# Performance work log

Measured on AMD Instinct MI355X. Metric: run time of the kernel, lower is better.

## Reference

```python
import jax, jax.numpy as jnp
import numpy as np

BIT, ROW, COL = 4, 8, 8
Y_ROW, Z_COL, K = 128, 128, 256  # inter_dimension = 256, K8 = 32
K8 = K // 8
BATCH, SEQ = 8, 2048


def _unpack_bits(packed, n_bits):
    """Unpack uint8 along last axis, big-endian (MSB first), matching np.packbits."""
    shifts = jnp.arange(7, -1, -1, dtype=jnp.uint8)
    bits = (packed[..., None] >> shifts) & jnp.uint8(1)  # [..., k8, 8]
    return bits.reshape(*packed.shape[:-1], -1)[..., :n_bits]


def setup_inputs() -> dict:
    rng = np.random.default_rng(0)
    # Generate underlying binary tensors so Y_sum / Z_sum are consistent with packed bits.
    Yb = rng.integers(0, 2, size=(BIT, ROW, COL, Y_ROW, K), dtype=np.uint8)
    Zb = rng.integers(0, 2, size=(BIT, ROW, COL, K, Z_COL), dtype=np.uint8)
    Y_packed = np.packbits(Yb, axis=-1)                                # [BIT,ROW,COL,Y_ROW,K8]
    Z_packed = np.packbits(Zb.transpose(0, 1, 2, 4, 3), axis=-1)        # [BIT,ROW,COL,Z_COL,K8]
    Y_sum = Yb.sum(axis=-1, keepdims=True).astype(np.int32)             # [BIT,ROW,COL,Y_ROW,1]
    Z_sum = Zb.sum(axis=-2, keepdims=True).astype(np.int32)             # [BIT,ROW,COL,1,Z_COL]

    key = jax.random.key(0)
    k1, k2, k3, k4, k5, k6 = jax.random.split(key, 6)
    X = jax.random.normal(k1, (BATCH, SEQ, COL * Z_COL), dtype=jnp.float32)
    a = jax.random.normal(k2, (BIT, 1, 1, 1, 1), dtype=jnp.float32) * 0.1
    b = jax.random.normal(k3, (BIT, 1, 1, 1, 1), dtype=jnp.float32) * 0.1
    c = jax.random.normal(k4, (BIT, 1, 1, 1, 1), dtype=jnp.float32) * 0.1
    d = jax.random.normal(k5, (1, 1, 1, 1), dtype=jnp.float32) * 0.1
    bias = jax.random.normal(k6, (ROW * Y_ROW,), dtype=jnp.float32) * 0.1
    return {
        "X": X,
        "Y_packed": jnp.asarray(Y_packed),
        "Z_packed": jnp.asarray(Z_packed),
        "Y_sum": jnp.asarray(Y_sum),
        "Z_sum": jnp.asarray(Z_sum),
        "a": a, "b": b, "c": c, "d": d, "bias": bias,
    }


def reference(X, Y_packed, Z_packed, Y_sum, Z_sum, a, b, c, d, bias):
    dtype = X.dtype
    # Unpack bits (fallback path of _matmul_via_unpack) and do binary matmul.
    Y = _unpack_bits(Y_packed, K).astype(dtype)        # [BIT,ROW,COL,Y_ROW,K]
    Zt = _unpack_bits(Z_packed, K).astype(dtype)       # [BIT,ROW,COL,Z_COL,K]
    W_core = jnp.einsum('brcyk,brczk->brcyz', Y, Zt)   # [BIT,ROW,COL,Y_ROW,Z_COL]
    # Affine recombination over bit planes.
    W = a * W_core + b * Y_sum.astype(dtype) + c * Z_sum.astype(dtype)
    W = W.sum(axis=0) + d                               # [ROW,COL,Y_ROW,Z_COL]
    W = W.transpose(0, 2, 1, 3).reshape(ROW * Y_ROW, COL * Z_COL)
    return X @ W.T + bias
```

## Files before the change

### kernel.cpp

```cpp
#include <hip/hip_runtime.h>
#include <hip/hip_bf16.h>
#include <stdint.h>

typedef unsigned int u32;
typedef unsigned short u16;
typedef __attribute__((ext_vector_type(8))) short short8;
typedef __attribute__((ext_vector_type(4))) float floatx4;

#define N_DIM 1024
#define K_DIM 1024
#define M_DIM 16384
#define EPW  68

__device__ __forceinline__ u32 pack4(uint4 v) {
    return (v.x & 0xffu) | ((v.y & 0xffu) << 8) | ((v.z & 0xffu) << 16) | (v.w << 24);
}

__device__ __forceinline__ u16 bf16rne(float f) {
    u32 u = __float_as_uint(f);
    return (u16)((u + 0x7fffu + ((u >> 16) & 1u)) >> 16);
}

__device__ __forceinline__ void load16_lds(const void* g, void* l) {
    __builtin_amdgcn_global_load_lds(
        (const __attribute__((address_space(1))) void*)g,
        (__attribute__((address_space(3))) void*)l, 16, 0, 0);
}

__global__ __launch_bounds__(256) void build_w(
        const u32* __restrict__ yp, const u32* __restrict__ zp,
        const int* __restrict__ ysum, const int* __restrict__ zsum,
        const float* __restrict__ pa, const float* __restrict__ pb,
        const float* __restrict__ pc, const float* __restrict__ pd,
        __hip_bfloat16* __restrict__ Wb) {
    __shared__ u32 sY[4096];
    __shared__ u32 sZ[1024];
    __shared__ int sYs[512];
    __shared__ int sZs[128];

    const int tid = threadIdx.x;
    const int rc = blockIdx.x >> 2;
    const int zq = blockIdx.x & 3;
    const int r = rc >> 3, c = rc & 7;
    const int z0 = zq * 32;

    const uint4 d0 = ((const uint4*)yp)[0], d1 = ((const uint4*)yp)[1];
    const int sdet = __popc(d0.x) + __popc(d0.y) + __popc(d0.z) + __popc(d0.w)
                   + __popc(d1.x) + __popc(d1.y) + __popc(d1.z) + __popc(d1.w);
    const bool widened = (sdet != ysum[0]);

    if (!widened) {
#pragma unroll
        for (int j = 0; j < 4; ++j) {
            const int chunk = tid + j * 256;
            const int f = chunk * 4;
            const int bit = f >> 10, rem = f & 1023;
            const u32 gw = (u32)((bit * 64 + r * 8 + c) * 1024 + rem);
            ((uint4*)sY)[chunk] = *(const uint4*)(yp + gw);
        }
        {
            const int f = tid * 4;
            const int bit = f >> 8;
            const u32 gw = (u32)((bit * 64 + r * 8 + c) * 1024 + z0 * 8 + (f & 255));
            ((uint4*)sZ)[tid] = *(const uint4*)(zp + gw);
        }
    } else {
#pragma unroll
        for (int j = 0; j < 4; ++j) {
            const int chunk = tid + j * 256;
            const int f = chunk * 4;
            const int bit = f >> 10, rem = f & 1023;
            const u32 gw = (u32)((bit * 64 + r * 8 + c) * 1024 + rem);
            uint4 o;
            o.x = pack4(((const uint4*)yp)[gw + 0]);
            o.y = pack4(((const uint4*)yp)[gw + 1]);
            o.z = pack4(((const uint4*)yp)[gw + 2]);
            o.w = pack4(((const uint4*)yp)[gw + 3]);
            ((uint4*)sY)[chunk] = o;
        }
        {
            const int f = tid * 4;
            const int bit = f >> 8;
            const u32 gw = (u32)((bit * 64 + r * 8 + c) * 1024 + z0 * 8 + (f & 255));
            uint4 o;
            o.x = pack4(((const uint4*)zp)[gw + 0]);
            o.y = pack4(((const uint4*)zp)[gw + 1]);
            o.z = pack4(((const uint4*)zp)[gw + 2]);
            o.w = pack4(((const uint4*)zp)[gw + 3]);
            ((uint4*)sZ)[tid] = o;
        }
    }
    for (int j = tid; j < 512; j += 256) {
        const int bit = j >> 7, y = j & 127;
        sYs[j] = ysum[((bit * 8 + r) * 8 + c) * 128 + y];
    }
    if (tid < 128) {
        const int bit = tid >> 5, zl = tid & 31;
        sZs[tid] = zsum[((bit * 8 + r) * 8 + c) * 128 + z0 + zl];
    }
    __syncthreads();

    float av[4], bv[4], cv[4];
#pragma unroll
    for (int bit = 0; bit < 4; ++bit) { av[bit] = pa[bit]; bv[bit] = pb[bit]; cv[bit] = pc[bit]; }
    const float dv = pd[0];

    const int y = tid & 127;
    const int zh = tid >> 7;

    u32 yw[4][8];
    float base = dv;
#pragma unroll
    for (int bit = 0; bit < 4; ++bit) {
        const uint4 q0 = ((const uint4*)sY)[bit * 256 + y * 2];
        const uint4 q1 = ((const uint4*)sY)[bit * 256 + y * 2 + 1];
        yw[bit][0] = q0.x; yw[bit][1] = q0.y; yw[bit][2] = q0.z; yw[bit][3] = q0.w;
        yw[bit][4] = q1.x; yw[bit][5] = q1.y; yw[bit][6] = q1.z; yw[bit][7] = q1.w;
        base += bv[bit] * (float)sYs[bit * 128 + y];
    }

    const int m = r * 128 + y;
#pragma unroll
    for (int zl2 = 0; zl2 < 16; ++zl2) {
        const int zl = zh * 16 + zl2;
        float wv = base;
#pragma unroll
        for (int bit = 0; bit < 4; ++bit) {
            const uint4 zw0 = ((const uint4*)sZ)[bit * 64 + zl * 2];
            const uint4 zw1 = ((const uint4*)sZ)[bit * 64 + zl * 2 + 1];
            int p = 0;
            p += __popc(yw[bit][0] & zw0.x);
            p += __popc(yw[bit][1] & zw0.y);
            p += __popc(yw[bit][2] & zw0.z);
            p += __popc(yw[bit][3] & zw0.w);
            p += __popc(yw[bit][4] & zw1.x);
            p += __popc(yw[bit][5] & zw1.y);
            p += __popc(yw[bit][6] & zw1.z);
            p += __popc(yw[bit][7] & zw1.w);
            wv += av[bit] * (float)p + cv[bit] * (float)sZs[bit * 32 + zl];
        }
        const int k = c * 128 + z0 + zl;
        Wb[(size_t)m * K_DIM + k] = __float2bfloat16(wv);
    }
}

__global__ __launch_bounds__(256) void convert_x(const float4* __restrict__ X,
                                                 ushort4* __restrict__ Xb) {
    const size_t base = (size_t)blockIdx.x * 512;
    const int tid = threadIdx.x;
    const float4 a = X[base + tid];
    const float4 b = X[base + 256 + tid];
    ushort4 oa, ob;
    oa.x = bf16rne(a.x); oa.y = bf16rne(a.y); oa.z = bf16rne(a.z); oa.w = bf16rne(a.w);
    ob.x = bf16rne(b.x); ob.y = bf16rne(b.y); ob.z = bf16rne(b.z); ob.w = bf16rne(b.w);
    Xb[base + tid] = oa;
    Xb[base + 256 + tid] = ob;
}

__global__ __launch_bounds__(512, 4) void gemm_bias(
        const u16* __restrict__ Xb, const u16* __restrict__ Wb,
        const float* __restrict__ bias, float* __restrict__ out) {
    __shared__ char lds[49152];
    char* As = lds;
    char* Bs = lds + 32768;

    const int tid = threadIdx.x;
    const int lane = tid & 63;
    const int w = tid >> 6;
    const int wr = w >> 1;
    const int wc = w & 1;
    const int mtile = blockIdx.x;
    const int ntile = blockIdx.y;
    const int m0 = mtile * 256, n0 = ntile * 128;

    const int lrow = lane >> 3;
    const int lkc  = (lane & 7) ^ lrow;
    const int fm = lane & 15, fq = lane >> 4;
    const int cx0 = ((0 + fq) ^ (fm & 7)) * 16;
    const int cx1 = ((4 + fq) ^ (fm & 7)) * 16;

    floatx4 acc[4][4] = {};

    for (int kt = 0; kt < K_DIM / 64; ++kt) {
        __syncthreads();
#pragma unroll
        for (int j = 0; j < 4; ++j) {
            const int cw = j * 8 + w;
            const int row = cw * 8 + lrow;
            load16_lds(Xb + (size_t)(m0 + row) * K_DIM + kt * 64 + lkc * 8,
                       As + cw * 1024 + lane * 16);
        }
#pragma unroll
        for (int j = 0; j < 2; ++j) {
            const int cw = j * 8 + w;
            const int row = cw * 8 + lrow;
            load16_lds(Wb + (size_t)(n0 + row) * K_DIM + kt * 64 + lkc * 8,
                       Bs + cw * 1024 + lane * 16);
        }
        __syncthreads();

#pragma unroll
        for (int kk = 0; kk < 2; ++kk) {
            const int cx = kk ? cx1 : cx0;
            short8 afr[4], bfr[4];
#pragma unroll
            for (int mi = 0; mi < 4; ++mi)
                afr[mi] = *(const short8*)(As + (wr * 64 + mi * 16 + fm) * 128 + cx);
#pragma unroll
            for (int ni = 0; ni < 4; ++ni)
                bfr[ni] = *(const short8*)(Bs + (wc * 64 + ni * 16 + fm) * 128 + cx);
#pragma unroll
            for (int mi = 0; mi < 4; ++mi)
#pragma unroll
                for (int ni = 0; ni < 4; ++ni)
                    acc[mi][ni] = __builtin_amdgcn_mfma_f32_16x16x32_bf16(
                        afr[mi], bfr[ni], acc[mi][ni], 0, 0, 0);
        }
    }

    float bias_r[4];
#pragma unroll
    for (int ni = 0; ni < 4; ++ni)
        bias_r[ni] = bias[n0 + wc * 64 + ni * 16 + fm];

    __syncthreads();
    float* ep = (float*)lds + w * (16 * EPW);
    const int gm0 = m0 + wr * 64;
    const int gn0 = n0 + wc * 64;

#pragma unroll
    for (int mi = 0; mi < 4; ++mi) {
#pragma unroll
        for (int ni = 0; ni < 4; ++ni)
#pragma unroll
            for (int reg = 0; reg < 4; ++reg)
                ep[(fq * 4 + reg) * EPW + ni * 16 + fm] = acc[mi][ni][reg] + bias_r[ni];
#pragma unroll
        for (int t = 0; t < 4; ++t) {
            const int lr = t * 4 + fq;
            const float4 v = *(const float4*)(ep + lr * EPW + fm * 4);
            *(float4*)(out + (size_t)(gm0 + mi * 16 + lr) * N_DIM + gn0 + fm * 4) = v;
        }
    }
}

extern "C" void kernel_launch(void* const* d_in, const int* in_sizes, int n_in,
                              void* d_out, int out_size, void* d_ws, size_t ws_size,
                              hipStream_t stream) {
    const float* X   = (const float*)d_in[0];
    const u32*   Yp  = (const u32*)d_in[1];
    const u32*   Zp  = (const u32*)d_in[2];
    const int*   Ys  = (const int*)d_in[3];
    const int*   Zs  = (const int*)d_in[4];
    const float* pa  = (const float*)d_in[5];
    const float* pb  = (const float*)d_in[6];
    const float* pc  = (const float*)d_in[7];
    const float* pd  = (const float*)d_in[8];
    const float* bias = (const float*)d_in[9];
    float* out = (float*)d_out;

    char* ws = (char*)d_ws;
    __hip_bfloat16* Wb = (__hip_bfloat16*)ws;
    u16*            Xb = (u16*)(ws + (2u << 20));

    build_w<<<256, 256, 0, stream>>>(Yp, Zp, Ys, Zs, pa, pb, pc, pd, Wb);
    convert_x<<<8192, 256, 0, stream>>>((const float4*)X, (ushort4*)Xb);
    gemm_bias<<<dim3(64, 8), 512, 0, stream>>>(Xb, (const u16*)Wb, bias, out);
}
```

Before: 172.3 us.

## Enlarge GEMM tile to 256x256 and double-buffer LDS with async prefetch

The GEMM block tile grows from 256x128 to 256x256, so each wave computes a 128x64 sub-tile with 32 accumulators. K-tiles are now double-buffered in 128 KB of dynamic LDS, with the next tile's global-to-LDS loads issued while the current one is being computed. The aim is more operand reuse per load and hidden global memory latency. The cost is higher register and LDS use, which limits occupancy to about one block per CU, and only 256 blocks are launched.

```diff
diff --git a/kernel.cpp b/kernel.cpp
--- a/kernel.cpp
+++ b/kernel.cpp
@@ -157,21 +157,18 @@
     Xb[base + 256 + tid] = ob;
 }
 
-__global__ __launch_bounds__(512, 4) void gemm_bias(
+__global__ __launch_bounds__(512, 2) void gemm_bias(
         const u16* __restrict__ Xb, const u16* __restrict__ Wb,
         const float* __restrict__ bias, float* __restrict__ out) {
-    __shared__ char lds[49152];
-    char* As = lds;
-    char* Bs = lds + 32768;
+    extern __shared__ char lds[];
 
     const int tid = threadIdx.x;
     const int lane = tid & 63;
     const int w = tid >> 6;
-    const int wr = w >> 1;
-    const int wc = w & 1;
-    const int mtile = blockIdx.x;
-    const int ntile = blockIdx.y;
-    const int m0 = mtile * 256, n0 = ntile * 128;
+    const int wr = w >> 2;
+    const int wc = w & 3;
+    const int m0 = blockIdx.x * 256;
+    const int n0 = blockIdx.y * 256;
 
     const int lrow = lane >> 3;
     const int lkc  = (lane & 7) ^ lrow;
@@ -179,44 +176,74 @@
     const int cx0 = ((0 + fq) ^ (fm & 7)) * 16;
     const int cx1 = ((4 + fq) ^ (fm & 7)) * 16;
 
-    floatx4 acc[4][4] = {};
-
-    for (int kt = 0; kt < K_DIM / 64; ++kt) {
-        __syncthreads();
-#pragma unroll
-        for (int j = 0; j < 4; ++j) {
-            const int cw = j * 8 + w;
-            const int row = cw * 8 + lrow;
-            load16_lds(Xb + (size_t)(m0 + row) * K_DIM + kt * 64 + lkc * 8,
-                       As + cw * 1024 + lane * 16);
-        }
-#pragma unroll
-        for (int j = 0; j < 2; ++j) {
-            const int cw = j * 8 + w;
-            const int row = cw * 8 + lrow;
-            load16_lds(Wb + (size_t)(n0 + row) * K_DIM + kt * 64 + lkc * 8,
-                       Bs + cw * 1024 + lane * 16);
-        }
-        __syncthreads();
-
-#pragma unroll
-        for (int kk = 0; kk < 2; ++kk) {
-            const int cx = kk ? cx1 : cx0;
-            short8 afr[4], bfr[4];
-#pragma unroll
-            for (int mi = 0; mi < 4; ++mi)
-                afr[mi] = *(const short8*)(As + (wr * 64 + mi * 16 + fm) * 128 + cx);
+#define STAGE(kt, s) do {                                                      \
+    char* As_ = lds + (s) * 65536;                                             \
+    char* Bs_ = lds + (s) * 65536 + 32768;                                     \
+    _Pragma("unroll")                                                          \
+    for (int j = 0; j < 4; ++j) {                                              \
+        const int cw = j * 8 + w;                       \
+        const int row = cw * 8 + lrow;                             \
+        load16_lds(Xb + (size_t)(m0 + row) * K_DIM + (kt) * 64 + lkc * 8,      \
+                   As_ + cw * 1024 + lane * 16);                               \
+    }                                                                          \
+    _Pragma("unroll")                                                          \
+    for (int j = 0; j < 4; ++j) {                                              \
+        const int cw = j * 8 + w;                                              \
+        const int row = cw * 8 + lrow;                             \
+        load16_lds(Wb + (size_t)(n0 + row) * K_DIM + (kt) * 64 + lkc * 8,      \
+                   Bs_ + cw * 1024 + lane * 16);                               \
+    }                                                                          \
+} while (0)
+
+    floatx4 acc[8][4] = {};
+
+    STAGE(0, 0);
+    STAGE(1, 1);
+
+    for (int kt = 0; kt < 16; ++kt) {
+        const int s = kt & 1;
+        if (kt < 15) asm volatile("s_waitcnt vmcnt(8)" ::: "memory");
+        else         asm volatile("s_waitcnt vmcnt(0)" ::: "memory");
+        __builtin_amdgcn_s_barrier();
+        asm volatile("" ::: "memory");
+
+        const char* Ab = lds + s * 65536;
+        const char* Bb = lds + s * 65536 + 32768;
+
+        short8 a0[8], b0[4];
+#pragma unroll
+        for (int mi = 0; mi < 8; ++mi)
+            a0[mi] = *(const short8*)(Ab + (wr * 128 + mi * 16 + fm) * 128 + cx0);
+#pragma unroll
+        for (int ni = 0; ni < 4; ++ni)
+            b0[ni] = *(const short8*)(Bb + (wc * 64 + ni * 16 + fm) * 128 + cx0);
+#pragma unroll
+        for (int mi = 0; mi < 8; ++mi)
 #pragma unroll
             for (int ni = 0; ni < 4; ++ni)
-                bfr[ni] = *(const short8*)(Bs + (wc * 64 + ni * 16 + fm) * 128 + cx);
-#pragma unroll
-            for (int mi = 0; mi < 4; ++mi)
-#pragma unroll
-                for (int ni = 0; ni < 4; ++ni)
-                    acc[mi][ni] = __builtin_amdgcn_mfma_f32_16x16x32_bf16(
-                        afr[mi], bfr[ni], acc[mi][ni], 0, 0, 0);
-        }
-    }
+                acc[mi][ni] = __builtin_amdgcn_mfma_f32_16x16x32_bf16(
+                    a0[mi], b0[ni], acc[mi][ni], 0, 0, 0);
+
+        short8 a1[8], b1[4];
+#pragma unroll
+        for (int mi = 0; mi < 8; ++mi)
+            a1[mi] = *(const short8*)(Ab + (wr * 128 + mi * 16 + fm) * 128 + cx1);
+#pragma unroll
+        for (int ni = 0; ni < 4; ++ni)
+            b1[ni] = *(const short8*)(Bb + (wc * 64 + ni * 16 + fm) * 128 + cx1);
+#pragma unroll
+        for (int mi = 0; mi < 8; ++mi)
+#pragma unroll
+            for (int ni = 0; ni < 4; ++ni)
+                acc[mi][ni] = __builtin_amdgcn_mfma_f32_16x16x32_bf16(
+                    a1[mi], b1[ni], acc[mi][ni], 0, 0, 0);
+
+        asm volatile("" ::: "memory");
+        __builtin_amdgcn_s_barrier();
+        asm volatile("" ::: "memory");
+        if (kt < 14) STAGE(kt + 2, s);
+    }
+#undef STAGE
 
     float bias_r[4];
 #pragma unroll
@@ -225,11 +252,11 @@
 
     __syncthreads();
     float* ep = (float*)lds + w * (16 * EPW);
-    const int gm0 = m0 + wr * 64;
+    const int gm0 = m0 + wr * 128;
     const int gn0 = n0 + wc * 64;
 
 #pragma unroll
-    for (int mi = 0; mi < 4; ++mi) {
+    for (int mi = 0; mi < 8; ++mi) {
 #pragma unroll
         for (int ni = 0; ni < 4; ++ni)
 #pragma unroll
@@ -263,7 +290,14 @@
     __hip_bfloat16* Wb = (__hip_bfloat16*)ws;
     u16*            Xb = (u16*)(ws + (2u << 20));
 
+    static bool attr_set = false;
+    if (!attr_set) {
+        hipFuncSetAttribute((const void*)gemm_bias,
+                            hipFuncAttributeMaxDynamicSharedMemorySize, 131072);
+        attr_set = true;
+    }
+
     build_w<<<256, 256, 0, stream>>>(Yp, Zp, Ys, Zs, pa, pb, pc, pd, Wb);
     convert_x<<<8192, 256, 0, stream>>>((const float4*)X, (ushort4*)Xb);
-    gemm_bias<<<dim3(64, 8), 512, 0, stream>>>(Xb, (const u16*)Wb, bias, out);
-}
+    gemm_bias<<<dim3(64, 4), 512, 131072, stream>>>(Xb, (const u16*)Wb, bias, out);
+}
```

Result: no change. 172.7 us (+0.2%).

## Double-buffer GEMM with phased MFMA schedule, larger tiles, and fused prep kernels

Applied to the files above, without the earlier changes.

Merges the W-building and X-conversion kernels into one launch so there is one fewer kernel boundary. The GEMM moves to 256x256 tiles with each wave computing 128x64, and uses two 64KB LDS slots filled by async global-to-LDS loads. The K loop is split into four barrier-separated MFMA phases with s_setprio, and the next tile's loads are issued inside those phases so memory latency hides behind compute. This costs 128KB of dynamic LDS and more accumulator registers, which lowers occupancy and leaves 256 blocks for the GEMM.

```diff
diff --git a/kernel.cpp b/kernel.cpp
--- a/kernel.cpp
+++ b/kernel.cpp
@@ -27,18 +27,32 @@
         (__attribute__((address_space(3))) void*)l, 16, 0, 0);
 }
 
-__global__ __launch_bounds__(256) void build_w(
+__global__ __launch_bounds__(256) void prep(
         const u32* __restrict__ yp, const u32* __restrict__ zp,
         const int* __restrict__ ysum, const int* __restrict__ zsum,
         const float* __restrict__ pa, const float* __restrict__ pb,
         const float* __restrict__ pc, const float* __restrict__ pd,
-        __hip_bfloat16* __restrict__ Wb) {
+        __hip_bfloat16* __restrict__ Wb,
+        const float4* __restrict__ X, ushort4* __restrict__ Xb) {
     __shared__ u32 sY[4096];
     __shared__ u32 sZ[1024];
     __shared__ int sYs[512];
     __shared__ int sZs[128];
 
     const int tid = threadIdx.x;
+
+    if (blockIdx.x >= 256) {
+        const size_t base = (size_t)(blockIdx.x - 256) * 512;
+        const float4 a = X[base + tid];
+        const float4 b = X[base + 256 + tid];
+        ushort4 oa, ob;
+        oa.x = bf16rne(a.x); oa.y = bf16rne(a.y); oa.z = bf16rne(a.z); oa.w = bf16rne(a.w);
+        ob.x = bf16rne(b.x); ob.y = bf16rne(b.y); ob.z = bf16rne(b.z); ob.w = bf16rne(b.w);
+        Xb[base + tid] = oa;
+        Xb[base + 256 + tid] = ob;
+        return;
+    }
+
     const int rc = blockIdx.x >> 2;
     const int zq = blockIdx.x & 3;
     const int r = rc >> 3, c = rc & 7;
@@ -144,34 +158,109 @@
     }
 }
 
-__global__ __launch_bounds__(256) void convert_x(const float4* __restrict__ X,
-                                                 ushort4* __restrict__ Xb) {
-    const size_t base = (size_t)blockIdx.x * 512;
-    const int tid = threadIdx.x;
-    const float4 a = X[base + tid];
-    const float4 b = X[base + 256 + tid];
-    ushort4 oa, ob;
-    oa.x = bf16rne(a.x); oa.y = bf16rne(a.y); oa.z = bf16rne(a.z); oa.w = bf16rne(a.w);
-    ob.x = bf16rne(b.x); ob.y = bf16rne(b.y); ob.z = bf16rne(b.z); ob.w = bf16rne(b.w);
-    Xb[base + tid] = oa;
-    Xb[base + 256 + tid] = ob;
-}
-
-__global__ __launch_bounds__(512, 4) void gemm_bias(
+__device__ __forceinline__ void stage_a(const u16* __restrict__ Xb, int m0, int kt,
+                                        char* SB, int w, int lane, int lrow, int lkc) {
+#pragma unroll
+    for (int j = 0; j < 4; ++j) {
+        const int cw = j * 8 + w;
+        const int row = cw * 8 + lrow;
+        load16_lds(Xb + (size_t)(m0 + row) * K_DIM + kt * 64 + lkc * 8,
+                   SB + cw * 1024 + lane * 16);
+    }
+}
+__device__ __forceinline__ void stage_b(const u16* __restrict__ Wb, int n0, int kt,
+                                        char* SB, int w, int lane, int lrow, int lkc) {
+#pragma unroll
+    for (int j = 0; j < 4; ++j) {
+        const int cw = j * 8 + w;
+        const int row = cw * 8 + lrow;
+        load16_lds(Wb + (size_t)(n0 + row) * K_DIM + kt * 64 + lkc * 8,
+                   SB + 32768 + cw * 1024 + lane * 16);
+    }
+}
+
+template<bool DO_STAGE, int VM>
+__device__ __forceinline__ void tile_phases(
+        const char* __restrict__ A_, const char* __restrict__ B_, char* SBst, int ktg,
+        floatx4 (&acc)[8][4],
+        const u16* __restrict__ Xb, const u16* __restrict__ Wb,
+        int m0, int n0, int w, int lane, int lrow, int lkc,
+        int wr, int wc, int fm, int cx0, int cx1) {
+    short8 a0[8], a1[8], b0[4], b1[4];
+
+#pragma unroll
+    for (int mi = 0; mi < 8; ++mi)
+        a0[mi] = *(const short8*)(A_ + (wr * 128 + mi * 16 + fm) * 128 + cx0);
+#pragma unroll
+    for (int ni = 0; ni < 4; ++ni)
+        b0[ni] = *(const short8*)(B_ + (wc * 64 + ni * 16 + fm) * 128 + cx0);
+    asm volatile("s_waitcnt lgkmcnt(8)" ::: "memory");
+    __builtin_amdgcn_s_barrier();
+    asm volatile("s_waitcnt lgkmcnt(0)" ::: "memory");
+    __builtin_amdgcn_s_setprio(1);
+#pragma unroll
+    for (int mi = 0; mi < 8; ++mi) {
+        acc[mi][0] = __builtin_amdgcn_mfma_f32_16x16x32_bf16(a0[mi], b0[0], acc[mi][0], 0, 0, 0);
+        acc[mi][1] = __builtin_amdgcn_mfma_f32_16x16x32_bf16(a0[mi], b0[1], acc[mi][1], 0, 0, 0);
+    }
+    __builtin_amdgcn_s_setprio(0);
+    __builtin_amdgcn_s_barrier();
+
+#pragma unroll
+    for (int ni = 0; ni < 4; ++ni)
+        b1[ni] = *(const short8*)(B_ + (wc * 64 + ni * 16 + fm) * 128 + cx1);
+    __builtin_amdgcn_s_barrier();
+    asm volatile("s_waitcnt lgkmcnt(0)" ::: "memory");
+    __builtin_amdgcn_s_setprio(1);
+#pragma unroll
+    for (int mi = 0; mi < 8; ++mi) {
+        acc[mi][2] = __builtin_amdgcn_mfma_f32_16x16x32_bf16(a0[mi], b0[2], acc[mi][2], 0, 0, 0);
+        acc[mi][3] = __builtin_amdgcn_mfma_f32_16x16x32_bf16(a0[mi], b0[3], acc[mi][3], 0, 0, 0);
+    }
+    __builtin_amdgcn_s_setprio(0);
+    __builtin_amdgcn_s_barrier();
+
+#pragma unroll
+    for (int mi = 0; mi < 8; ++mi)
+        a1[mi] = *(const short8*)(A_ + (wr * 128 + mi * 16 + fm) * 128 + cx1);
+    if (DO_STAGE) stage_b(Wb, n0, ktg, SBst, w, lane, lrow, lkc);
+    __builtin_amdgcn_s_barrier();
+    asm volatile("s_waitcnt lgkmcnt(0)" ::: "memory");
+    __builtin_amdgcn_s_setprio(1);
+#pragma unroll
+    for (int mi = 0; mi < 8; ++mi) {
+        acc[mi][0] = __builtin_amdgcn_mfma_f32_16x16x32_bf16(a1[mi], b1[0], acc[mi][0], 0, 0, 0);
+        acc[mi][1] = __builtin_amdgcn_mfma_f32_16x16x32_bf16(a1[mi], b1[1], acc[mi][1], 0, 0, 0);
+    }
+    __builtin_amdgcn_s_setprio(0);
+    __builtin_amdgcn_s_barrier();
+
+    if (DO_STAGE) stage_a(Xb, m0, ktg, SBst, w, lane, lrow, lkc);
+    if (VM == 8)      asm volatile("s_waitcnt vmcnt(8)" ::: "memory");
+    else if (VM == 0) asm volatile("s_waitcnt vmcnt(0)" ::: "memory");
+    __builtin_amdgcn_s_barrier();
+    __builtin_amdgcn_s_setprio(1);
+#pragma unroll
+    for (int mi = 0; mi < 8; ++mi) {
+        acc[mi][2] = __builtin_amdgcn_mfma_f32_16x16x32_bf16(a1[mi], b1[2], acc[mi][2], 0, 0, 0);
+        acc[mi][3] = __builtin_amdgcn_mfma_f32_16x16x32_bf16(a1[mi], b1[3], acc[mi][3], 0, 0, 0);
+    }
+    __builtin_amdgcn_s_setprio(0);
+    __builtin_amdgcn_s_barrier();
+}
+
+__global__ __launch_bounds__(512, 2) void gemm_bias(
         const u16* __restrict__ Xb, const u16* __restrict__ Wb,
         const float* __restrict__ bias, float* __restrict__ out) {
-    __shared__ char lds[49152];
-    char* As = lds;
-    char* Bs = lds + 32768;
+    extern __shared__ char lds[];
 
     const int tid = threadIdx.x;
     const int lane = tid & 63;
     const int w = tid >> 6;
-    const int wr = w >> 1;
-    const int wc = w & 1;
-    const int mtile = blockIdx.x;
-    const int ntile = blockIdx.y;
-    const int m0 = mtile * 256, n0 = ntile * 128;
+    const int wr = w >> 2;
+    const int wc = w & 3;
+    const int m0 = blockIdx.x * 256;
+    const int n0 = blockIdx.y * 256;
 
     const int lrow = lane >> 3;
     const int lkc  = (lane & 7) ^ lrow;
@@ -179,44 +268,28 @@
     const int cx0 = ((0 + fq) ^ (fm & 7)) * 16;
     const int cx1 = ((4 + fq) ^ (fm & 7)) * 16;
 
-    floatx4 acc[4][4] = {};
-
-    for (int kt = 0; kt < K_DIM / 64; ++kt) {
-        __syncthreads();
-#pragma unroll
-        for (int j = 0; j < 4; ++j) {
-            const int cw = j * 8 + w;
-            const int row = cw * 8 + lrow;
-            load16_lds(Xb + (size_t)(m0 + row) * K_DIM + kt * 64 + lkc * 8,
-                       As + cw * 1024 + lane * 16);
-        }
-#pragma unroll
-        for (int j = 0; j < 2; ++j) {
-            const int cw = j * 8 + w;
-            const int row = cw * 8 + lrow;
-            load16_lds(Wb + (size_t)(n0 + row) * K_DIM + kt * 64 + lkc * 8,
-                       Bs + cw * 1024 + lane * 16);
-        }
-        __syncthreads();
-
-#pragma unroll
-        for (int kk = 0; kk < 2; ++kk) {
-            const int cx = kk ? cx1 : cx0;
-            short8 afr[4], bfr[4];
-#pragma unroll
-            for (int mi = 0; mi < 4; ++mi)
-                afr[mi] = *(const short8*)(As + (wr * 64 + mi * 16 + fm) * 128 + cx);
-#pragma unroll
-            for (int ni = 0; ni < 4; ++ni)
-                bfr[ni] = *(const short8*)(Bs + (wc * 64 + ni * 16 + fm) * 128 + cx);
-#pragma unroll
-            for (int mi = 0; mi < 4; ++mi)
-#pragma unroll
-                for (int ni = 0; ni < 4; ++ni)
-                    acc[mi][ni] = __builtin_amdgcn_mfma_f32_16x16x32_bf16(
-                        afr[mi], bfr[ni], acc[mi][ni], 0, 0, 0);
-        }
-    }
+    char* slot0 = lds;
+    char* slot1 = lds + 65536;
+
+    floatx4 acc[8][4] = {};
+
+    stage_b(Wb, n0, 0, slot0, w, lane, lrow, lkc);
+    stage_a(Xb, m0, 0, slot0, w, lane, lrow, lkc);
+    stage_b(Wb, n0, 1, slot1, w, lane, lrow, lkc);
+    stage_a(Xb, m0, 1, slot1, w, lane, lrow, lkc);
+    asm volatile("s_waitcnt vmcnt(8)" ::: "memory");
+    __builtin_amdgcn_s_barrier();
+
+    for (int it = 0; it < 7; ++it) {
+        tile_phases<true, 8>(slot0, slot0 + 32768, slot0, 2 * it + 2, acc,
+                             Xb, Wb, m0, n0, w, lane, lrow, lkc, wr, wc, fm, cx0, cx1);
+        tile_phases<true, 8>(slot1, slot1 + 32768, slot1, 2 * it + 3, acc,
+                             Xb, Wb, m0, n0, w, lane, lrow, lkc, wr, wc, fm, cx0, cx1);
+    }
+    tile_phases<false, 0>(slot0, slot0 + 32768, slot0, 0, acc,
+                          Xb, Wb, m0, n0, w, lane, lrow, lkc, wr, wc, fm, cx0, cx1);
+    tile_phases<false, -1>(slot1, slot1 + 32768, slot1, 0, acc,
+                           Xb, Wb, m0, n0, w, lane, lrow, lkc, wr, wc, fm, cx0, cx1);
 
     float bias_r[4];
 #pragma unroll
@@ -225,11 +298,11 @@
 
     __syncthreads();
     float* ep = (float*)lds + w * (16 * EPW);
-    const int gm0 = m0 + wr * 64;
+    const int gm0 = m0 + wr * 128;
     const int gn0 = n0 + wc * 64;
 
 #pragma unroll
-    for (int mi = 0; mi < 4; ++mi) {
+    for (int mi = 0; mi < 8; ++mi) {
 #pragma unroll
         for (int ni = 0; ni < 4; ++ni)
 #pragma unroll
@@ -263,7 +336,14 @@
     __hip_bfloat16* Wb = (__hip_bfloat16*)ws;
     u16*            Xb = (u16*)(ws + (2u << 20));
 
-    build_w<<<256, 256, 0, stream>>>(Yp, Zp, Ys, Zs, pa, pb, pc, pd, Wb);
-    convert_x<<<8192, 256, 0, stream>>>((const float4*)X, (ushort4*)Xb);
-    gemm_bias<<<dim3(64, 8), 512, 0, stream>>>(Xb, (const u16*)Wb, bias, out);
-}
+    static bool attr_set = false;
+    if (!attr_set) {
+        hipFuncSetAttribute((const void*)gemm_bias,
+                            hipFuncAttributeMaxDynamicSharedMemorySize, 131072);
+        attr_set = true;
+    }
+
+    prep<<<8448, 256, 0, stream>>>(Yp, Zp, Ys, Zs, pa, pb, pc, pd, Wb,
+                                   (const float4*)X, (ushort4*)Xb);
+    gemm_bias<<<dim3(64, 4), 512, 131072, stream>>>(Xb, (const u16*)Wb, bias, out);
+}
```

Measured after the change: 169.7 us. Within noise of the previous version (-1.5%).

## Double-buffer GEMM K-loop with async LDS loads and merge prep kernels

Applied to the files above, without the earlier changes.

The GEMM now uses two LDS slots with K-step 32 and 4 waves per block, each wave computing a 128x64 tile. Global-to-LDS loads for the next stage are issued between MFMA halves, with explicit vmcnt waits, barriers and setprio, so memory traffic overlaps compute. The W-build and X-conversion kernels are merged into one launch to save a launch and let the two kinds of work run concurrently. The cost is higher register pressure from the 8x4 accumulators and more fragile hand-written synchronisation.

```diff
diff --git a/kernel.cpp b/kernel.cpp
--- a/kernel.cpp
+++ b/kernel.cpp
@@ -27,18 +27,32 @@
         (__attribute__((address_space(3))) void*)l, 16, 0, 0);
 }
 
-__global__ __launch_bounds__(256) void build_w(
+__global__ __launch_bounds__(256) void prep(
         const u32* __restrict__ yp, const u32* __restrict__ zp,
         const int* __restrict__ ysum, const int* __restrict__ zsum,
         const float* __restrict__ pa, const float* __restrict__ pb,
         const float* __restrict__ pc, const float* __restrict__ pd,
-        __hip_bfloat16* __restrict__ Wb) {
+        __hip_bfloat16* __restrict__ Wb,
+        const float4* __restrict__ X, ushort4* __restrict__ Xb) {
     __shared__ u32 sY[4096];
     __shared__ u32 sZ[1024];
     __shared__ int sYs[512];
     __shared__ int sZs[128];
 
     const int tid = threadIdx.x;
+
+    if (blockIdx.x >= 256) {
+        const size_t base = (size_t)(blockIdx.x - 256) * 512;
+        const float4 a = X[base + tid];
+        const float4 b = X[base + 256 + tid];
+        ushort4 oa, ob;
+        oa.x = bf16rne(a.x); oa.y = bf16rne(a.y); oa.z = bf16rne(a.z); oa.w = bf16rne(a.w);
+        ob.x = bf16rne(b.x); ob.y = bf16rne(b.y); ob.z = bf16rne(b.z); ob.w = bf16rne(b.w);
+        Xb[base + tid] = oa;
+        Xb[base + 256 + tid] = ob;
+        return;
+    }
+
     const int rc = blockIdx.x >> 2;
     const int zq = blockIdx.x & 3;
     const int r = rc >> 3, c = rc & 7;
@@ -144,79 +158,103 @@
     }
 }
 
-__global__ __launch_bounds__(256) void convert_x(const float4* __restrict__ X,
-                                                 ushort4* __restrict__ Xb) {
-    const size_t base = (size_t)blockIdx.x * 512;
-    const int tid = threadIdx.x;
-    const float4 a = X[base + tid];
-    const float4 b = X[base + 256 + tid];
-    ushort4 oa, ob;
-    oa.x = bf16rne(a.x); oa.y = bf16rne(a.y); oa.z = bf16rne(a.z); oa.w = bf16rne(a.w);
-    ob.x = bf16rne(b.x); ob.y = bf16rne(b.y); ob.z = bf16rne(b.z); ob.w = bf16rne(b.w);
-    Xb[base + tid] = oa;
-    Xb[base + 256 + tid] = ob;
-}
-
-__global__ __launch_bounds__(512, 4) void gemm_bias(
+__device__ __forceinline__ void stage32(const u16* __restrict__ Xb,
+        const u16* __restrict__ Wb, int m0, int n0, int kt, char* slot,
+        int w, int lane, int srow, int csrc) {
+#pragma unroll
+    for (int j = 0; j < 4; ++j) {
+        const int slab = w * 4 + j;
+        const int row = slab * 16 + srow;
+        load16_lds(Xb + (size_t)(m0 + row) * K_DIM + kt * 32 + csrc * 8,
+                   slot + slab * 1024 + lane * 16);
+    }
+#pragma unroll
+    for (int j = 0; j < 2; ++j) {
+        const int slab = w * 2 + j;
+        const int row = slab * 16 + srow;
+        load16_lds(Wb + (size_t)(n0 + row) * K_DIM + kt * 32 + csrc * 8,
+                   slot + 16384 + slab * 1024 + lane * 16);
+    }
+}
+
+template<bool DO_STAGE, int VM>
+__device__ __forceinline__ void tile32(const char* __restrict__ slot,
+        char* stslot, int ktg, floatx4 (&acc)[8][4],
+        const u16* __restrict__ Xb, const u16* __restrict__ Wb,
+        int m0, int n0, int w, int lane, int srow, int csrc,
+        int wr, int wc, int fm, int cx) {
+    const char* As = slot;
+    const char* Bs = slot + 16384;
+    short8 a[8], b[4];
+
+#pragma unroll
+    for (int mi = 0; mi < 8; ++mi)
+        a[mi] = *(const short8*)(As + (wr * 128 + mi * 16 + fm) * 64 + cx);
+#pragma unroll
+    for (int ni = 0; ni < 4; ++ni)
+        b[ni] = *(const short8*)(Bs + (wc * 64 + ni * 16 + fm) * 64 + cx);
+    __builtin_amdgcn_s_barrier();
+    asm volatile("s_waitcnt lgkmcnt(0)" ::: "memory");
+    __builtin_amdgcn_s_setprio(1);
+#pragma unroll
+    for (int mi = 0; mi < 8; ++mi) {
+        acc[mi][0] = __builtin_amdgcn_mfma_f32_16x16x32_bf16(a[mi], b[0], acc[mi][0], 0, 0, 0);
+        acc[mi][1] = __builtin_amdgcn_mfma_f32_16x16x32_bf16(a[mi], b[1], acc[mi][1], 0, 0, 0);
+    }
+    __builtin_amdgcn_s_setprio(0);
+    __builtin_amdgcn_s_barrier();
+
+    if (DO_STAGE) stage32(Xb, Wb, m0, n0, ktg, stslot, w, lane, srow, csrc);
+    if (VM == 6)      asm volatile("s_waitcnt vmcnt(6)" ::: "memory");
+    else              asm volatile("s_waitcnt vmcnt(0)" ::: "memory");
+    __builtin_amdgcn_s_barrier();
+    __builtin_amdgcn_s_setprio(1);
+#pragma unroll
+    for (int mi = 0; mi < 8; ++mi) {
+        acc[mi][2] = __builtin_amdgcn_mfma_f32_16x16x32_bf16(a[mi], b[2], acc[mi][2], 0, 0, 0);
+        acc[mi][3] = __builtin_amdgcn_mfma_f32_16x16x32_bf16(a[mi], b[3], acc[mi][3], 0, 0, 0);
+    }
+    __builtin_amdgcn_s_setprio(0);
+    __builtin_amdgcn_s_barrier();
+}
+
+__global__ __launch_bounds__(256, 2) void gemm_bias(
         const u16* __restrict__ Xb, const u16* __restrict__ Wb,
         const float* __restrict__ bias, float* __restrict__ out) {
     __shared__ char lds[49152];
-    char* As = lds;
-    char* Bs = lds + 32768;
 
     const int tid = threadIdx.x;
     const int lane = tid & 63;
     const int w = tid >> 6;
     const int wr = w >> 1;
     const int wc = w & 1;
-    const int mtile = blockIdx.x;
-    const int ntile = blockIdx.y;
-    const int m0 = mtile * 256, n0 = ntile * 128;
-
-    const int lrow = lane >> 3;
-    const int lkc  = (lane & 7) ^ lrow;
+    const int m0 = blockIdx.x * 256;
+    const int n0 = blockIdx.y * 128;
+
+    const int srow = lane >> 2;
+    const int csrc = (lane & 3) ^ ((lane >> 3) & 3);
     const int fm = lane & 15, fq = lane >> 4;
-    const int cx0 = ((0 + fq) ^ (fm & 7)) * 16;
-    const int cx1 = ((4 + fq) ^ (fm & 7)) * 16;
-
-    floatx4 acc[4][4] = {};
-
-    for (int kt = 0; kt < K_DIM / 64; ++kt) {
-        __syncthreads();
-#pragma unroll
-        for (int j = 0; j < 4; ++j) {
-            const int cw = j * 8 + w;
-            const int row = cw * 8 + lrow;
-            load16_lds(Xb + (size_t)(m0 + row) * K_DIM + kt * 64 + lkc * 8,
-                       As + cw * 1024 + lane * 16);
-        }
-#pragma unroll
-        for (int j = 0; j < 2; ++j) {
-            const int cw = j * 8 + w;
-            const int row = cw * 8 + lrow;
-            load16_lds(Wb + (size_t)(n0 + row) * K_DIM + kt * 64 + lkc * 8,
-                       Bs + cw * 1024 + lane * 16);
-        }
-        __syncthreads();
-
-#pragma unroll
-        for (int kk = 0; kk < 2; ++kk) {
-            const int cx = kk ? cx1 : cx0;
-            short8 afr[4], bfr[4];
-#pragma unroll
-            for (int mi = 0; mi < 4; ++mi)
-                afr[mi] = *(const short8*)(As + (wr * 64 + mi * 16 + fm) * 128 + cx);
-#pragma unroll
-            for (int ni = 0; ni < 4; ++ni)
-                bfr[ni] = *(const short8*)(Bs + (wc * 64 + ni * 16 + fm) * 128 + cx);
-#pragma unroll
-            for (int mi = 0; mi < 4; ++mi)
-#pragma unroll
-                for (int ni = 0; ni < 4; ++ni)
-                    acc[mi][ni] = __builtin_amdgcn_mfma_f32_16x16x32_bf16(
-                        afr[mi], bfr[ni], acc[mi][ni], 0, 0, 0);
-        }
-    }
+    const int cx = (fq ^ ((fm >> 1) & 3)) * 16;
+
+    char* slot0 = lds;
+    char* slot1 = lds + 24576;
+
+    floatx4 acc[8][4] = {};
+
+    stage32(Xb, Wb, m0, n0, 0, slot0, w, lane, srow, csrc);
+    stage32(Xb, Wb, m0, n0, 1, slot1, w, lane, srow, csrc);
+    __syncthreads();
+
+    for (int it = 0; it < 15; ++it) {
+        tile32<true, 6>(slot0, slot0, 2 * it + 2, acc, Xb, Wb, m0, n0,
+                        w, lane, srow, csrc, wr, wc, fm, cx);
+        tile32<true, 6>(slot1, slot1, 2 * it + 3, acc, Xb, Wb, m0, n0,
+                        w, lane, srow, csrc, wr, wc, fm, cx);
+    }
+    tile32<false, 0>(slot0, slot0, 0, acc, Xb, Wb, m0, n0,
+                     w, lane, srow, csrc, wr, wc, fm, cx);
+    tile32<false, 0>(slot1, slot1, 0, acc, Xb, Wb, m0, n0,
+                     w, lane, srow, csrc, wr, wc, fm, cx);
 
     float bias_r[4];
 #pragma unroll
@@ -225,11 +263,11 @@
 
     __syncthreads();
     float* ep = (float*)lds + w * (16 * EPW);
-    const int gm0 = m0 + wr * 64;
+    const int gm0 = m0 + wr * 128;
     const int gn0 = n0 + wc * 64;
 
 #pragma unroll
-    for (int mi = 0; mi < 4; ++mi) {
+    for (int mi = 0; mi < 8; ++mi) {
 #pragma unroll
         for (int ni = 0; ni < 4; ++ni)
 #pragma unroll
@@ -263,7 +301,7 @@
     __hip_bfloat16* Wb = (__hip_bfloat16*)ws;
     u16*            Xb = (u16*)(ws + (2u << 20));
 
-    build_w<<<256, 256, 0, stream>>>(Yp, Zp, Ys, Zs, pa, pb, pc, pd, Wb);
-    convert_x<<<8192, 256, 0, stream>>>((const float4*)X, (ushort4*)Xb);
-    gemm_bias<<<dim3(64, 8), 512, 0, stream>>>(Xb, (const u16*)Wb, bias, out);
-}
+    prep<<<8448, 256, 0, stream>>>(Yp, Zp, Ys, Zs, pa, pb, pc, pd, Wb,
+                                   (const float4*)X, (ushort4*)Xb);
+    gemm_bias<<<dim3(64, 8), 256, 0, stream>>>(Xb, (const u16*)Wb, bias, out);
+}
```

Result: no change. 169.6 us (-1.6%).
